# Kernel optimization log

Measured on AMD Instinct MI355X. Metric: run time of the kernel, lower is better.

## Reference

```python
import jax, jax.numpy as jnp
import numpy as np

N_HEAD = 16
N_KV_HEAD = 8
HEAD_DIM = 128
BLOCK_SIZE = 2048


def _rope_cache(T, hd):
    # faithful to torch: freqs repeat_interleave(2) along last dim
    inv_freq = 1.0 / (10000.0 ** (jnp.arange(0, hd, 2, dtype=jnp.float32) / hd))
    t = jnp.arange(T, dtype=jnp.float32)
    freqs = jnp.outer(t, inv_freq)            # [T, hd/2]
    freqs = jnp.repeat(freqs, 2, axis=-1)     # [T, hd]
    return jnp.cos(freqs), jnp.sin(freqs)


def _apply_rope(x, cos, sin):
    # x: [B, H, T, hd]; rotate-half convention from the torch code
    hd = x.shape[-1]
    x1, x2 = x[..., : hd // 2], x[..., hd // 2 :]
    x_rot = jnp.concatenate([-x2, x1], axis=-1)
    return x * cos + x_rot * sin


def setup_inputs() -> dict:
    key = jax.random.key(0)
    ks = jax.random.split(key, 5)
    B, T, C = 4, 2048, 2048
    kv_dim = N_KV_HEAD * HEAD_DIM
    s = 0.02
    return {
        "x": jax.random.normal(ks[0], (B, T, C), dtype=jnp.float32),
        "Wq": jax.random.normal(ks[1], (C, C), dtype=jnp.float32) * s,
        "Wk": jax.random.normal(ks[2], (kv_dim, C), dtype=jnp.float32) * s,
        "Wv": jax.random.normal(ks[3], (kv_dim, C), dtype=jnp.float32) * s,
        "Wo": jax.random.normal(ks[4], (C, C), dtype=jnp.float32) * s,
    }


def reference(x, Wq, Wk, Wv, Wo):
    B, T, C = x.shape
    hd = HEAD_DIM
    # projections (torch Linear: x @ W.T)
    q = (x @ Wq.T).reshape(B, T, N_HEAD, hd).transpose(0, 2, 1, 3)      # [B,H,T,hd]
    k = (x @ Wk.T).reshape(B, T, N_KV_HEAD, hd).transpose(0, 2, 1, 3)   # [B,Hkv,T,hd]
    v = (x @ Wv.T).reshape(B, T, N_KV_HEAD, hd).transpose(0, 2, 1, 3)

    cos, sin = _rope_cache(T, hd)  # start_pos = 0
    q = _apply_rope(q, cos, sin)
    k = _apply_rope(k, cos, sin)

    # GQA: repeat kv heads
    rep = N_HEAD // N_KV_HEAD
    k = jnp.repeat(k, rep, axis=1)  # [B,H,T,hd]
    v = jnp.repeat(v, rep, axis=1)

    scale = 1.0 / jnp.sqrt(jnp.float32(hd))
    scores = jnp.einsum("bhqd,bhkd->bhqk", q, k) * scale
    causal = jnp.tril(jnp.ones((T, T), dtype=bool))
    scores = jnp.where(causal, scores, jnp.finfo(scores.dtype).min)
    attn = jax.nn.softmax(scores, axis=-1)
    out = jnp.einsum("bhqk,bhkd->bhqd", attn, v)  # [B,H,T,hd]

    y = out.transpose(0, 2, 1, 3).reshape(B, T, C)
    return y @ Wo.T
```

## Files before the change

kernel.cpp:

```cpp
#include <hip/hip_runtime.h>

#define SCALE 0.08838834764831845f

typedef unsigned short bfu;
typedef __attribute__((ext_vector_type(8))) short bf16x8;
typedef __attribute__((ext_vector_type(4))) float f32x4;
typedef __attribute__((ext_vector_type(16))) float f32x16;

__device__ __forceinline__ unsigned short f2bf(float f) {
  unsigned int u = __float_as_uint(f);
  u += 0x7FFFu + ((u >> 16) & 1u);
  return (unsigned short)(u >> 16);
}
__device__ __forceinline__ float bf2f(unsigned short h) {
  return __uint_as_float(((unsigned int)h) << 16);
}
__device__ __forceinline__ unsigned int cvtpk(float a, float b) {
  unsigned int r;
  asm("v_cvt_pk_bf16_f32 %0, %1, %2" : "=v"(r) : "v"(a), "v"(b));
  return r;
}
__device__ __forceinline__ void pl32swap(unsigned int& a, unsigned int& b) {
  asm volatile("v_permlane32_swap_b32 %0, %1" : "+v"(a), "+v"(b));
}
__device__ __forceinline__ void async16(const void* g, void* l) {
  __builtin_amdgcn_global_load_lds(
      (const __attribute__((address_space(1))) unsigned int*)g,
      (__attribute__((address_space(3))) unsigned int*)l, 16, 0, 0);
}
__device__ __forceinline__ void barrier_sb() {
  __builtin_amdgcn_sched_barrier(0);
  __builtin_amdgcn_s_barrier();
  __builtin_amdgcn_sched_barrier(0);
}
__device__ __forceinline__ void wait0_bar() {
  __builtin_amdgcn_sched_barrier(0);
  asm volatile("s_waitcnt vmcnt(0)" ::: "memory");
  __builtin_amdgcn_s_barrier();
  __builtin_amdgcn_sched_barrier(0);
}

__global__ __launch_bounds__(256) void cvt_bf16(const float* __restrict__ src,
                                                bfu* __restrict__ dst, int n4) {
  int i = blockIdx.x * 256 + threadIdx.x;
  if (i >= n4) return;
  float4 v = ((const float4*)src)[i];
  ushort4 o;
  o.x = f2bf(v.x); o.y = f2bf(v.y); o.z = f2bf(v.z); o.w = f2bf(v.w);
  ((ushort4*)dst)[i] = o;
}

__global__ __launch_bounds__(256) void rope_table(float2* __restrict__ tab) {
  int idx = blockIdx.x * 256 + threadIdx.x;
  int t = idx >> 6, f = idx & 63;
  const float nl = -0.14391156463f;
  float th = (float)t * expf((float)f * nl);
  tab[idx] = make_float2(cosf(th), sinf(th));
}

__device__ __forceinline__ void storeC(float* p, float v) { *p = v; }
__device__ __forceinline__ void storeC(bfu* p, float v) { *p = f2bf(v); }

template <typename OutT, bool FUSE>
__global__ __launch_bounds__(512, 2) void gemm256(
    const bfu* __restrict__ A, const bfu* __restrict__ B,
    OutT* __restrict__ C, const float2* __restrict__ ropeTab,
    bfu* __restrict__ qTo, bfu* __restrict__ kTo, bfu* __restrict__ vTo,
    int M, int N, int K) {
  __shared__ __align__(16) char smem[131072];
  const int tid = threadIdx.x;
  const int w = tid >> 6, l = tid & 63;
  const int lr = l & 15, lg = l >> 4;
  const int wr = w >> 2, wc = w & 3;

  const int nm = gridDim.x, nn = gridDim.y;
  const int flat = blockIdx.y * nm + blockIdx.x;
  const int xcd = flat & 7, j = flat >> 3;
  const int RM = (nm * nn) >> 5;
  const int nregm = nm / RM;
  const int m0 = ((xcd % nregm) * RM + (j >> 2)) * 256;
  const int n0 = ((xcd / nregm) * 4 + (j & 3)) * 256;

  const int sr = l >> 3;
  const int sc = (l & 7) ^ sr;
  auto stageHalf = [&](const bfu* G, int grow0, int kcol, char* lds) {
#pragma unroll
    for (int jj = 0; jj < 2; jj++) {
      int row = (jj * 8 + w) * 8 + sr;
      async16(G + (size_t)(grow0 + row) * K + kcol + sc * 8,
              lds + (jj * 8 + w) * 1024 + l * 16);
    }
  };

  f32x4 acc[8][4];
#pragma unroll
  for (int i = 0; i < 8; i++)
#pragma unroll
    for (int jj = 0; jj < 4; jj++) acc[i][jj] = (f32x4){0.f, 0.f, 0.f, 0.f};

  stageHalf(A, m0, 0, smem);
  stageHalf(A, m0 + 128, 0, smem + 16384);
  stageHalf(B, n0, 0, smem + 65536);
  stageHalf(B, n0 + 128, 0, smem + 65536 + 16384);

  const int KT = K >> 6;
  const int swiz = (lr & 7) << 4;
  const int cbase = (wc >> 1) * 128 + (wc & 1) * 32;
#pragma unroll 1
  for (int t = 0; t < KT; t++) {
    const int bt = t & 1;
    const char* Ah = smem + bt * 32768 + wr * 16384;
    const char* Bt = smem + 65536 + bt * 32768;
    char* An = smem + (bt ^ 1) * 32768;
    char* Bn = smem + 65536 + (bt ^ 1) * 32768;
    const bool pfch = (t + 1 < KT);
    const int kn = (t + 1) << 6;

    if (pfch) {
      stageHalf(A, m0, kn, An);
      asm volatile("s_waitcnt vmcnt(2)" ::: "memory");
    } else {
      asm volatile("s_waitcnt vmcnt(0)" ::: "memory");
    }
    barrier_sb();

    bf16x8 bfr[4][2];
#pragma unroll
    for (int n = 0; n < 4; n++) {
      const char* rowp =
          Bt + (cbase + (n & 1) * 16 + (n >> 1) * 64 + lr) * 128;
#pragma unroll
      for (int s = 0; s < 2; s++)
        bfr[n][s] = *(const bf16x8*)(rowp + ((((s << 2) + lg) << 4) ^ swiz));
    }

#pragma unroll
    for (int p = 0; p < 4; p++) {
      bf16x8 af[2][2];
#pragma unroll
      for (int m2 = 0; m2 < 2; m2++) {
        const char* rowp = Ah + ((p * 2 + m2) * 16 + lr) * 128;
#pragma unroll
        for (int s = 0; s < 2; s++)
          af[m2][s] = *(const bf16x8*)(rowp + ((((s << 2) + lg) << 4) ^ swiz));
      }
      if (pfch) {
        if (p == 1) stageHalf(A, m0 + 128, kn, An + 16384);
        if (p == 2) stageHalf(B, n0, kn, Bn);
        if (p == 3) stageHalf(B, n0 + 128, kn, Bn + 16384);
      }
      __builtin_amdgcn_s_setprio(1);
#pragma unroll
      for (int m2 = 0; m2 < 2; m2++)
#pragma unroll
        for (int n = 0; n < 4; n++)
#pragma unroll
          for (int s = 0; s < 2; s++)
            acc[p * 2 + m2][n] = __builtin_amdgcn_mfma_f32_16x16x32_bf16(
                af[m2][s], bfr[n][s], acc[p * 2 + m2][n], 0, 0, 0);
      __builtin_amdgcn_s_setprio(0);
    }
    barrier_sb();
  }

  if constexpr (!FUSE) {
#pragma unroll
    for (int i = 0; i < 8; i++)
#pragma unroll
      for (int jj = 0; jj < 4; jj++)
#pragma unroll
        for (int r = 0; r < 4; r++) {
          int gm = m0 + wr * 128 + i * 16 + lg * 4 + r;
          int gn = n0 + cbase + (jj & 1) * 16 + (jj >> 1) * 64 + lr;
          storeC(&C[(size_t)gm * N + gn], acc[i][jj][r]);
        }
  } else {
    const int head = (n0 >> 7) + (wc >> 1);
    if (head < 24) {
#pragma unroll
      for (int i = 0; i < 8; i++)
#pragma unroll
        for (int r = 0; r < 4; r++) {
          int gm = m0 + wr * 128 + i * 16 + lg * 4 + r;
          int tt = gm & 2047, bb = gm >> 11;
          bfu* rowp = (head < 16)
                          ? qTo + (((size_t)((bb * 16 + head) * 2048 + tt)) << 7)
                          : kTo + (((size_t)((bb * 8 + head - 16) * 2048 + tt)) << 7);
          const float2* trow = ropeTab + tt * 64;
#pragma unroll
          for (int n = 0; n < 2; n++) {
            int d = (wc & 1) * 32 + n * 16 + lr;
            int i1 = d >> 1;
            float2 cs1 = trow[i1];
            float2 cs2 = trow[i1 + 32];
            float x1 = acc[i][n][r], x2 = acc[i][n + 2][r];
            rowp[d] = f2bf(x1 * cs1.x - x2 * cs1.y);
            rowp[d + 64] = f2bf(x2 * cs2.x + x1 * cs2.y);
          }
        }
    } else {
      const int kh = head - 24;
#pragma unroll
      for (int i = 0; i < 8; i++) {
        int gm0 = m0 + wr * 128 + i * 16 + lg * 4;
        int t0 = gm0 & 2047, bb = gm0 >> 11;
#pragma unroll
        for (int n = 0; n < 4; n++) {
          int d = (wc & 1) * 32 + (n & 1) * 16 + (n >> 1) * 64 + lr;
          bfu* p = vTo + (((size_t)((bb * 8 + kh) * 128 + d)) << 11) + t0;
          ushort4 o;
          o.x = f2bf(acc[i][n][0]);
          o.y = f2bf(acc[i][n][1]);
          o.z = f2bf(acc[i][n][2]);
          o.w = f2bf(acc[i][n][3]);
          *(ushort4*)p = o;
        }
      }
    }
  }
}

__global__ __launch_bounds__(512, 2) void flash_attn7(const bfu* __restrict__ qT,
                                                      const bfu* __restrict__ kT,
                                                      const bfu* __restrict__ vT,
                                                      bfu* __restrict__ attn) {
  __shared__ __align__(16) char smem[65536];
  const int tid = threadIdx.x;
  const int w = tid >> 6, l = tid & 63;
  const int ln = l & 31, h2 = l >> 5;
  const int hsw = w >> 2, w4 = w & 3;
  const int idx = blockIdx.x;
  const int khb = idx & 31;
  const int pg = idx >> 5;
  const int kh = khb & 7, b = khb >> 3;
  const int hh = kh * 2 + hsw;
  const int nkbA = 2 * pg + 2;
  const int NT = 34;

  const bfu* Qh = qT + ((size_t)(b * 16 + hh) * 2048) * 128;
  const bfu* Kb = kT + ((size_t)(b * 8 + kh) * 2048) * 128;
  const bfu* Vb = vT + ((size_t)(b * 8 + kh) * 128) * 2048;

  auto stageK = [&](int buf, int t) {
    char* Kl = smem + buf * 16384;
    const bfu* src = Kb + (size_t)t * 64 * 128;
#pragma unroll
    for (int ii = 0; ii < 2; ii++) {
      int i = w * 2 + ii;
      int row = i * 4 + (l >> 4);
      int ck = (l & 15) ^ (row & 15);
      async16(src + row * 128 + ck * 8, Kl + i * 1024 + l * 16);
    }
  };
  auto stageV = [&](int buf, int t) {
    char* Vl = smem + 32768 + buf * 16384;
    const bfu* src = Vb + t * 64;
#pragma unroll
    for (int jj = 0; jj < 2; jj++) {
      int j = w * 2 + jj;
      int row = j * 8 + (l >> 3);
      int ck = (l & 7) ^ (row & 7);
      async16(src + (size_t)row * 2048 + ck * 8, Vl + j * 1024 + l * 16);
    }
  };

  int qrow0 = pg * 128 + w4 * 32;

  bf16x8 qf[8];
#pragma unroll
  for (int dt = 0; dt < 8; dt++)
    qf[dt] = *(const bf16x8*)(Qh + (size_t)(qrow0 + ln) * 128 + dt * 16 + h2 * 8);

  f32x16 O[4];
#pragma unroll
  for (int mt = 0; mt < 4; mt++)
#pragma unroll
    for (int r = 0; r < 16; r++) O[mt][r] = 0.f;
  float li = 0.f;

  auto flush = [&]() {
    float ls = li + __shfl_xor(li, 32);
    float inv = 1.f / ls;
    bfu* orow = attn + ((size_t)(b * 2048 + qrow0 + ln)) * 2048 + hh * 128;
#pragma unroll
    for (int mt = 0; mt < 4; mt++)
#pragma unroll
      for (int g = 0; g < 4; g++) {
        unsigned int r0 = cvtpk(O[mt][g * 4 + 0] * inv, O[mt][g * 4 + 1] * inv);
        unsigned int r1 = cvtpk(O[mt][g * 4 + 2] * inv, O[mt][g * 4 + 3] * inv);
        uint2 o; o.x = r0; o.y = r1;
        *(uint2*)(orow + mt * 32 + g * 8 + h2 * 4) = o;
      }
  };

  stageK(0, 0);
  stageV(0, 0);

#pragma unroll 1
  for (int t = 0; t < NT; t++) {
    wait0_bar();
    if (t + 1 < NT) {
      const int kn = (t + 1 >= nkbA) ? (t + 1 - nkbA) : (t + 1);
      stageK((t + 1) & 1, kn);
      stageV((t + 1) & 1, kn);
    }

    if (t == nkbA) {
      flush();
      qrow0 = (15 - pg) * 128 + w4 * 32;
#pragma unroll
      for (int dt = 0; dt < 8; dt++)
        qf[dt] =
            *(const bf16x8*)(Qh + (size_t)(qrow0 + ln) * 128 + dt * 16 + h2 * 8);
#pragma unroll
      for (int mt = 0; mt < 4; mt++)
#pragma unroll
        for (int r = 0; r < 16; r++) O[mt][r] = 0.f;
      li = 0.f;
    }

    const int k0 = ((t >= nkbA) ? (t - nkbA) : t) * 64;
    const int myrow = qrow0 + ln;
    if (k0 <= qrow0 + 31) {
      const char* Kl = smem + (t & 1) * 16384;
      const char* Vl = smem + 32768 + (t & 1) * 16384;

      f32x16 S0, S1;
#pragma unroll
      for (int r = 0; r < 16; r++) { S0[r] = 0.f; S1[r] = 0.f; }
      const int swk = (ln & 15) << 4;
      __builtin_amdgcn_s_setprio(1);
#pragma unroll
      for (int dt = 0; dt < 8; dt++) {
        bf16x8 kf0 =
            *(const bf16x8*)(Kl + ln * 256 + ((dt * 32 + h2 * 16) ^ swk));
        bf16x8 kf1 = *(const bf16x8*)(Kl + (32 + ln) * 256 +
                                      ((dt * 32 + h2 * 16) ^ swk));
        S0 = __builtin_amdgcn_mfma_f32_32x32x16_bf16(kf0, qf[dt], S0, 0, 0, 0);
        S1 = __builtin_amdgcn_mfma_f32_32x32x16_bf16(kf1, qf[dt], S1, 0, 0, 0);
      }
      __builtin_amdgcn_s_setprio(0);

      const bool need_mask = (k0 + 63) > qrow0;
      bf16x8 pfr[4];
#pragma unroll
      for (int half = 0; half < 2; half++) {
        float p[16];
#pragma unroll
        for (int r = 0; r < 16; r++) {
          float s = half ? S1[r] : S0[r];
          float pv = __builtin_exp2f(fmaf(s, 0.12751743f, -17.312340f));
          if (need_mask) {
            int key = k0 + half * 32 + (r & 3) + 8 * (r >> 2) + 4 * h2;
            if (key > myrow) pv = 0.f;
          }
          p[r] = pv;
          li += pv;
        }
#pragma unroll
        for (int kt = 0; kt < 2; kt++) {
          const float* q = p + kt * 8;
          unsigned int a0 = cvtpk(q[0], q[1]);
          unsigned int a1 = cvtpk(q[2], q[3]);
          unsigned int b0 = cvtpk(q[4], q[5]);
          unsigned int b1 = cvtpk(q[6], q[7]);
          pl32swap(a0, b0);
          pl32swap(a1, b1);
          union { unsigned int u[4]; bf16x8 v; } c;
          c.u[0] = a0; c.u[1] = a1; c.u[2] = b0; c.u[3] = b1;
          pfr[half * 2 + kt] = c.v;
        }
      }

      const int swv = (ln & 7) << 4;
      __builtin_amdgcn_s_setprio(1);
#pragma unroll
      for (int mt = 0; mt < 4; mt++) {
        const char* vb = Vl + (mt * 32 + ln) * 128;
#pragma unroll
        for (int kt = 0; kt < 4; kt++) {
          bf16x8 vf = *(const bf16x8*)(vb + ((kt * 32 + h2 * 16) ^ swv));
          O[mt] = __builtin_amdgcn_mfma_f32_32x32x16_bf16(vf, pfr[kt], O[mt], 0, 0, 0);
        }
      }
      __builtin_amdgcn_s_setprio(0);
    }
  }

  flush();
}

extern "C" void kernel_launch(void* const* d_in, const int* in_sizes, int n_in,
                              void* d_out, int out_size, void* d_ws, size_t ws_size,
                              hipStream_t stream) {
  const float* x = (const float*)d_in[0];
  const float* Wq = (const float*)d_in[1];
  const float* Wk = (const float*)d_in[2];
  const float* Wv = (const float*)d_in[3];
  const float* Wo = (const float*)d_in[4];
  float* out = (float*)d_out;
  char* ws = (char*)d_ws;

  bfu* xb     = (bfu*)(ws);
  bfu* Wqkv   = (bfu*)(ws + 33554432);
  bfu* Wob    = (bfu*)(ws + 50331648);
  float2* tab = (float2*)(ws + 58720256);
  bfu* qT     = (bfu*)(ws + 125829120);
  bfu* kT     = (bfu*)(ws + 159383552);
  bfu* vT     = (bfu*)(ws + 176160768);
  bfu* attn = xb;

  cvt_bf16<<<16384, 256, 0, stream>>>(x, xb, 4194304);
  cvt_bf16<<<4096, 256, 0, stream>>>(Wq, Wqkv, 1048576);
  cvt_bf16<<<2048, 256, 0, stream>>>(Wk, Wqkv + (size_t)2048 * 2048, 524288);
  cvt_bf16<<<2048, 256, 0, stream>>>(Wv, Wqkv + (size_t)3072 * 2048, 524288);
  cvt_bf16<<<4096, 256, 0, stream>>>(Wo, Wob, 1048576);
  rope_table<<<512, 256, 0, stream>>>(tab);

  gemm256<bfu, true><<<dim3(32, 16), 512, 0, stream>>>(
      xb, Wqkv, (bfu*)nullptr, tab, qT, kT, vT, 8192, 4096, 2048);
  flash_attn7<<<256, 512, 0, stream>>>(qT, kT, vT, attn);
  gemm256<float, false><<<dim3(32, 8), 512, 0, stream>>>(
      attn, Wob, out, nullptr, nullptr, nullptr, nullptr, 8192, 2048, 2048);
}
```

Before: 466.8 us.

## Replace output projection GEMM with 128x128-tile kernel and XCD-aware block mapping

Adds a dedicated 128x128-tile bf16 MFMA GEMM with double-buffered async LDS staging for the final output projection, replacing the 256x256-tile generic kernel. This raises the block count from 256 to 1024 so the GPU's compute units are better filled, and remaps blocks so neighbouring tiles land on the same XCD for cache locality. Smaller tiles mean less data reuse per block and more global/L2 traffic.

```diff
diff --git a/kernel.cpp b/kernel.cpp
--- a/kernel.cpp
+++ b/kernel.cpp
@@ -218,6 +218,105 @@
       }
     }
   }
+}
+
+__global__ __launch_bounds__(512, 2) void gemm128(const bfu* __restrict__ A,
+                                                  const bfu* __restrict__ B,
+                                                  float* __restrict__ C,
+                                                  int M, int N, int K) {
+  __shared__ __align__(16) char smem[65536];
+  const int tid = threadIdx.x;
+  const int w = tid >> 6, l = tid & 63;
+  const int lr = l & 15, lg = l >> 4;
+  const int wr = w >> 2, wc = w & 3;
+
+  const int nm = gridDim.x, nn = gridDim.y;
+  const int flat = blockIdx.y * nm + blockIdx.x;
+  const int xcd = flat & 7, j = flat >> 3;
+  const int RM = (nm * nn) >> 5;
+  const int nregm = nm / RM;
+  const int m0 = ((xcd % nregm) * RM + (j >> 2)) * 128;
+  const int n0 = ((xcd / nregm) * 4 + (j & 3)) * 128;
+
+  const int sr = l >> 3;
+  const int sc = (l & 7) ^ sr;
+  auto stageHalf = [&](const bfu* G, int grow0, int kcol, char* lds) {
+#pragma unroll
+    for (int jj = 0; jj < 2; jj++) {
+      int row = (jj * 8 + w) * 8 + sr;
+      async16(G + (size_t)(grow0 + row) * K + kcol + sc * 8,
+              lds + (jj * 8 + w) * 1024 + l * 16);
+    }
+  };
+
+  f32x4 acc[4][2];
+#pragma unroll
+  for (int i = 0; i < 4; i++)
+#pragma unroll
+    for (int n = 0; n < 2; n++) acc[i][n] = (f32x4){0.f, 0.f, 0.f, 0.f};
+
+  stageHalf(A, m0, 0, smem);
+  stageHalf(B, n0, 0, smem + 32768);
+
+  const int KT = K >> 6;
+  const int swiz = (lr & 7) << 4;
+#pragma unroll 1
+  for (int t = 0; t < KT; t++) {
+    const int bt = t & 1;
+    const char* Ah = smem + bt * 16384;
+    const char* Bt = smem + 32768 + bt * 16384;
+    char* An = smem + (bt ^ 1) * 16384;
+    char* Bn = smem + 32768 + (bt ^ 1) * 16384;
+    const bool pfch = (t + 1 < KT);
+    const int kn = (t + 1) << 6;
+
+    if (pfch) {
+      stageHalf(A, m0, kn, An);
+      asm volatile("s_waitcnt vmcnt(2)" ::: "memory");
+    } else {
+      asm volatile("s_waitcnt vmcnt(0)" ::: "memory");
+    }
+    barrier_sb();
+
+    bf16x8 bfr[2][2];
+#pragma unroll
+    for (int n = 0; n < 2; n++) {
+      const char* rowp = Bt + (wc * 32 + n * 16 + lr) * 128;
+#pragma unroll
+      for (int s = 0; s < 2; s++)
+        bfr[n][s] = *(const bf16x8*)(rowp + ((((s << 2) + lg) << 4) ^ swiz));
+    }
+
+#pragma unroll
+    for (int p = 0; p < 4; p++) {
+      bf16x8 af[2];
+      const char* rowp = Ah + (wr * 64 + p * 16 + lr) * 128;
+#pragma unroll
+      for (int s = 0; s < 2; s++)
+        af[s] = *(const bf16x8*)(rowp + ((((s << 2) + lg) << 4) ^ swiz));
+      if (p == 2 && pfch) stageHalf(B, n0, kn, Bn);
+      __builtin_amdgcn_s_setprio(1);
+#pragma unroll
+      for (int n = 0; n < 2; n++)
+#pragma unroll
+        for (int s = 0; s < 2; s++)
+          acc[p][n] = __builtin_amdgcn_mfma_f32_16x16x32_bf16(
+              af[s], bfr[n][s], acc[p][n], 0, 0, 0);
+      __builtin_amdgcn_s_setprio(0);
+    }
+    barrier_sb();
+  }
+
+#pragma unroll
+  for (int i = 0; i < 4; i++)
+#pragma unroll
+    for (int n = 0; n < 2; n++)
+#pragma unroll
+      for (int r = 0; r < 4; r++) {
+        int gm = m0 + wr * 64 + i * 16 + lg * 4 + r;
+        int gn = n0 + wc * 32 + n * 16 + lr;
+        C[(size_t)gm * N + gn] = acc[i][n][r];
+      }
 }
 
 __global__ __launch_bounds__(512, 2) void flash_attn7(const bfu* __restrict__ qT,
@@ -420,6 +519,5 @@
   gemm256<bfu, true><<<dim3(32, 16), 512, 0, stream>>>(
       xb, Wqkv, (bfu*)nullptr, tab, qT, kT, vT, 8192, 4096, 2048);
   flash_attn7<<<256, 512, 0, stream>>>(qT, kT, vT, attn);
-  gemm256<float, false><<<dim3(32, 8), 512, 0, stream>>>(
-      attn, Wob, out, nullptr, nullptr, nullptr, nullptr, 8192, 2048, 2048);
-}
+  gemm128<<<dim3(64, 16), 512, 0, stream>>>(attn, Wob, out, 8192, 2048, 2048);
+}
```

After: 468.3 us. Within noise of the previous version (+0.3%).
